# Optimization experiments

Hardware: AMD Instinct MI355X
Metric: run time of the kernel (lower is better)

Reference implementation:

```python
import jax, jax.numpy as jnp
import numpy as np

N, Q, K, L, H, C, B = 32768, 8192, 16, 8, 128, 20, 4
COS_EPS = 1e-8


def setup_inputs() -> dict:
    key = jax.random.key(0)
    ks = jax.random.split(key, 8)
    support_xyz = jax.random.normal(ks[0], (N, 3), jnp.float32)
    batch_index = jnp.sort(jax.random.randint(ks[1], (N,), 0, B))
    filtered_index = jnp.sort(jax.random.randint(ks[2], (Q,), 0, N))
    gcnfeat = jax.random.normal(ks[3], (N, H + C), jnp.float32)
    leaf_node_all = jax.random.normal(ks[4], (Q, L, 3 * H), jnp.float32)
    W1 = jax.random.normal(ks[5], (10, 64), jnp.float32) * 0.1
    b1 = jnp.zeros((64,), jnp.float32)
    W2 = jax.random.normal(ks[6], (64, H), jnp.float32) * 0.1
    b2 = jnp.zeros((H,), jnp.float32)
    Wl = jax.random.normal(ks[7], (C, H), jnp.float32) * 0.1
    bl = jnp.zeros((H,), jnp.float32)
    return dict(support_xyz=support_xyz, batch_index=batch_index,
                filtered_index=filtered_index, gcnfeat=gcnfeat,
                leaf_node_all=leaf_node_all, W1=W1, b1=b1, W2=W2, b2=b2,
                Wl=Wl, bl=bl)


def _cosine_aff(a, b):
    # a: [Q,L,H], b: [Q,K,H] -> [Q,L,K] cosine similarity matrix
    an = a / jnp.maximum(jnp.linalg.norm(a, axis=-1, keepdims=True), COS_EPS)
    bn = b / jnp.maximum(jnp.linalg.norm(b, axis=-1, keepdims=True), COS_EPS)
    return jnp.einsum('qlh,qkh->qlk', an, bn)


def _auction(mat):
    # Bertsekas auction algorithm (maximization LAP), mat: [L,K], K >= L.
    Lr, Kc = mat.shape
    eps = 1.0 / Lr
    col_ids = jnp.arange(Kc, dtype=jnp.int32)

    def cond(st):
        _, ass = st
        return jnp.any(ass < 0)

    def body(st):
        cost, ass = st
        unassigned = ass < 0                                   # [L]
        value = mat - cost[None, :]                            # [L,K]
        top2, top_idx = jax.lax.top_k(value, 2)
        bid_inc = jnp.where(unassigned, top2[:, 0] - top2[:, 1] + eps, 0.0)
        bids = jnp.zeros((Lr, Kc), mat.dtype).at[jnp.arange(Lr), top_idx[:, 0]].set(bid_inc)
        have_bid = jnp.any(bids > 0, axis=0)                   # [K]
        high_bid = jnp.max(bids, axis=0)                       # [K]
        high_bidder = jnp.argmax(bids, axis=0).astype(jnp.int32)
        cost = cost + jnp.where(have_bid, high_bid, 0.0)
        # kick out previous owners of columns that received bids
        kicked = (ass >= 0) & have_bid[jnp.clip(ass, 0, Kc - 1)]
        ass = jnp.where(kicked, -1, ass)
        # assign the high bidder of each bid-receiving column (others dropped OOB)
        tgt = jnp.where(have_bid, high_bidder, Lr)
        ass = ass.at[tgt].set(col_ids, mode='drop')
        return cost, ass

    cost0 = jnp.zeros((Kc,), mat.dtype)
    ass0 = jnp.full((Lr,), -1, jnp.int32)
    _, ass = jax.lax.while_loop(cond, body, (cost0, ass0))
    return ass


def reference(support_xyz, batch_index, filtered_index, gcnfeat, leaf_node_all,
              W1, b1, W2, b2, Wl, bl):
    query_xyz = support_xyz[filtered_index]                    # [Q,3]
    qb = batch_index[filtered_index]                           # [Q]
    # batched KNN: squared distances via GEMM form, mask cross-batch pairs
    d2 = (jnp.sum(query_xyz ** 2, -1)[:, None]
          + jnp.sum(support_xyz ** 2, -1)[None, :]
          - 2.0 * query_xyz @ support_xyz.T)                   # [Q,N]
    d2 = jnp.where(qb[:, None] == batch_index[None, :], d2, jnp.inf)
    _, col = jax.lax.top_k(-d2, K)                             # [Q,K]
    xyz_j = support_xyz[col]                                   # [Q,K,3]
    xyz_i = jnp.broadcast_to(query_xyz[:, None, :], xyz_j.shape)
    diff = xyz_i - xyz_j
    dist = jnp.linalg.norm(diff, axis=-1, keepdims=True)
    ew = jnp.concatenate([xyz_i, xyz_j, diff, dist], axis=-1)  # [Q,K,10]
    edge_w = jax.nn.relu(ew @ W1 + b1) @ W2 + b2               # [Q,K,H] rel_map
    feat_j = gcnfeat[col]                                      # [Q,K,H+C]
    cls_w = feat_j[..., -C:] @ Wl + bl                         # [Q,K,H] label_map
    m1 = _cosine_aff(leaf_node_all[:, :, :H], edge_w)
    m2 = _cosine_aff(leaf_node_all[:, :, H:2 * H], cls_w)
    m3 = _cosine_aff(leaf_node_all[:, :, 2 * H:], feat_j[..., :H])
    mat = (m1 + m2) / 4.0 + m3 / 2.0                           # [Q,L,K]
    gm_idx = jax.vmap(_auction)(jax.lax.stop_gradient(mat))    # [Q,L]
    scores = jnp.take_along_axis(mat, gm_idx[:, :, None].astype(jnp.int32), axis=2)[..., 0]
    return jnp.mean(scores, axis=-1)                           # [Q]
```

## Files before the change

kernel.cpp:

```cpp
#include <hip/hip_runtime.h>
#include <stdint.h>

#define KNN 16
#define LROWS 8
#define KBQ 8
#define KCAP 128

__device__ __forceinline__ void load4(const float* __restrict__ sxyz, int i0,
                                      int N, float px[4], float py[4],
                                      float pz[4]) {
  if (i0 + 4 <= N) {
    float4 v0 = *(const float4*)&sxyz[3 * i0];
    float4 v1 = *(const float4*)&sxyz[3 * i0 + 4];
    float4 v2 = *(const float4*)&sxyz[3 * i0 + 8];
    px[0] = v0.x; py[0] = v0.y; pz[0] = v0.z;
    px[1] = v0.w; py[1] = v1.x; pz[1] = v1.y;
    px[2] = v1.z; py[2] = v1.w; pz[2] = v2.x;
    px[3] = v2.y; py[3] = v2.z; pz[3] = v2.w;
  } else {
#pragma unroll
    for (int e = 0; e < 4; ++e) {
      int i = i0 + e; bool ok = i < N;
      px[e] = ok ? sxyz[3 * i] : 0.f;
      py[e] = ok ? sxyz[3 * i + 1] : 0.f;
      pz[e] = ok ? sxyz[3 * i + 2] : 0.f;
    }
  }
}

__global__ __launch_bounds__(256) void knn_kernel(
    const float* __restrict__ sxyz, const int* __restrict__ bidx,
    const int* __restrict__ fidx, int* __restrict__ col, int N, int Q) {
  const int t = threadIdx.x;
  const int qbase = blockIdx.x * KBQ;

  __shared__ float s_min[KBQ][256];
  __shared__ unsigned long long s_cand[KBQ][KCAP];
  __shared__ int s_cnt[KBQ];
  __shared__ float s_thr[KBQ];
  __shared__ float s_qx[KBQ], s_qy[KBQ], s_qz[KBQ];
  __shared__ int s_lo[KBQ], s_hi[KBQ];

  if (t < 2 * KBQ) {
    int qi = qbase + (t & (KBQ - 1));
    if (qi < Q) {
      int fi = fidx[qi];
      int qb = bidx[fi];
      if (t < KBQ) {
        s_qx[t] = sxyz[3 * fi]; s_qy[t] = sxyz[3 * fi + 1]; s_qz[t] = sxyz[3 * fi + 2];
        int a = 0, b = N;
        while (a < b) { int m = (a + b) >> 1; if (bidx[m] < qb) a = m + 1; else b = m; }
        s_lo[t] = a;
      } else {
        int a = 0, b = N;
        while (a < b) { int m = (a + b) >> 1; if (bidx[m] <= qb) a = m + 1; else b = m; }
        s_hi[t - KBQ] = a;
      }
    } else {
      if (t < KBQ) { s_lo[t] = 0; s_qx[t] = s_qy[t] = s_qz[t] = 0.f; }
      else s_hi[t - KBQ] = 0;
    }
  }
  if (t < KBQ) s_cnt[t] = 0;
  __syncthreads();

  float qx[KBQ], qy[KBQ], qz[KBQ], qmin[KBQ];
  int qlo[KBQ], qhi[KBQ];
#pragma unroll
  for (int qi = 0; qi < KBQ; ++qi) {
    qx[qi] = s_qx[qi]; qy[qi] = s_qy[qi]; qz[qi] = s_qz[qi];
    qlo[qi] = s_lo[qi]; qhi[qi] = s_hi[qi];
    qmin[qi] = 3e38f;
  }
  int blo = qlo[0], bhi = qhi[0];
#pragma unroll
  for (int qi = 1; qi < KBQ; ++qi) { blo = min(blo, qlo[qi]); bhi = max(bhi, qhi[qi]); }
  const int base = blo & ~3;

  for (int i0 = base + 4 * t; i0 < bhi; i0 += 1024) {
    float px[4], py[4], pz[4];
    load4(sxyz, i0, N, px, py, pz);
#pragma unroll
    for (int e = 0; e < 4; ++e) {
      int i = i0 + e;
#pragma unroll
      for (int qi = 0; qi < KBQ; ++qi) {
        float dx = qx[qi] - px[e], dy = qy[qi] - py[e], dz = qz[qi] - pz[e];
        float d2 = fmaf(dx, dx, fmaf(dy, dy, dz * dz));
        bool v = (i >= qlo[qi]) && (i < qhi[qi]);
        qmin[qi] = fminf(qmin[qi], v ? d2 : 3e38f);
      }
    }
  }
#pragma unroll
  for (int qi = 0; qi < KBQ; ++qi) s_min[qi][t] = qmin[qi];
  __syncthreads();

  {
    int qi = t >> 5, u = t & 31;
    float v[8];
#pragma unroll
    for (int s = 0; s < 8; ++s) v[s] = s_min[qi][u + 32 * s];
    float thr = 3e38f;
    for (int r = 0; r < KNN; ++r) {
      float lm = fminf(fminf(fminf(v[0], v[1]), fminf(v[2], v[3])),
                       fminf(fminf(v[4], v[5]), fminf(v[6], v[7])));
      float gm = lm;
      gm = fminf(gm, __shfl_xor(gm, 1, 64));
      gm = fminf(gm, __shfl_xor(gm, 2, 64));
      gm = fminf(gm, __shfl_xor(gm, 4, 64));
      gm = fminf(gm, __shfl_xor(gm, 8, 64));
      gm = fminf(gm, __shfl_xor(gm, 16, 64));
      unsigned long long b = __ballot(lm == gm);
      unsigned mask = (unsigned)((b >> (t & 32)) & 0xffffffffull);
      int win = __ffs(mask) - 1;
      if (u == win) {
        if (v[0] == gm) v[0] = 3e38f; else if (v[1] == gm) v[1] = 3e38f;
        else if (v[2] == gm) v[2] = 3e38f; else if (v[3] == gm) v[3] = 3e38f;
        else if (v[4] == gm) v[4] = 3e38f; else if (v[5] == gm) v[5] = 3e38f;
        else if (v[6] == gm) v[6] = 3e38f; else v[7] = 3e38f;
      }
      thr = gm;
    }
    if (u == 0)
      s_thr[qi] = (s_hi[qi] - s_lo[qi] <= KCAP) ? 3e38f : thr;
  }
  __syncthreads();

  float qthr[KBQ];
#pragma unroll
  for (int qi = 0; qi < KBQ; ++qi) qthr[qi] = s_thr[qi];

  for (int i0 = base + 4 * t; i0 < bhi; i0 += 1024) {
    float px[4], py[4], pz[4];
    load4(sxyz, i0, N, px, py, pz);
#pragma unroll
    for (int e = 0; e < 4; ++e) {
      int i = i0 + e;
#pragma unroll
      for (int qi = 0; qi < KBQ; ++qi) {
        float dx = qx[qi] - px[e], dy = qy[qi] - py[e], dz = qz[qi] - pz[e];
        float d2 = fmaf(dx, dx, fmaf(dy, dy, dz * dz));
        if (i >= qlo[qi] && i < qhi[qi] && d2 <= qthr[qi]) {
          int pos = atomicAdd(&s_cnt[qi], 1);
          if (pos < KCAP)
            s_cand[qi][pos] =
                (((unsigned long long)__float_as_uint(d2)) << 32) | (unsigned)i;
        }
      }
    }
  }
  __syncthreads();

  {
    int qi = t >> 5, u = t & 31;
    int M = min(s_cnt[qi], KCAP);
    for (int r = 0; r < KNN; ++r) {
      unsigned long long lm = ~0ull; int ls = -1;
      for (int s = u; s < M; s += 32) {
        unsigned long long vv = s_cand[qi][s];
        if (vv < lm) { lm = vv; ls = s; }
      }
      unsigned long long gm = lm, o;
      o = __shfl_xor(gm, 1, 64); if (o < gm) gm = o;
      o = __shfl_xor(gm, 2, 64); if (o < gm) gm = o;
      o = __shfl_xor(gm, 4, 64); if (o < gm) gm = o;
      o = __shfl_xor(gm, 8, 64); if (o < gm) gm = o;
      o = __shfl_xor(gm, 16, 64); if (o < gm) gm = o;
      unsigned long long b = __ballot(lm == gm);
      unsigned mask = (unsigned)((b >> (t & 32)) & 0xffffffffull);
      int win = __ffs(mask) - 1;
      if (u == win && ls >= 0 && gm != ~0ull) {
        s_cand[qi][ls] = ~0ull;
        col[(size_t)(qbase + qi) * KNN + r] = (int)(unsigned)(gm & 0xffffffffull);
      }
    }
  }
}

#define OFF_LEAF 0
#define OFF_EDGE 3104
#define OFF_B 5184
#define OFF_EW 7264
#define OFF_FC 7456
#define S_TOTAL 7776

template <bool EXT>
__global__ __launch_bounds__(128) void fused_kernel(
    const float* __restrict__ sxyz,
    const int* __restrict__ fidx,
    const float* __restrict__ gcn,
    const float* __restrict__ leaf,
    const float* __restrict__ W1, const float* __restrict__ b1,
    const float* __restrict__ W2, const float* __restrict__ b2,
    const float* __restrict__ Wl, const float* __restrict__ bl,
    const int* __restrict__ col,
    float* __restrict__ matw, float* __restrict__ out) {
  const int q = blockIdx.x;
  const int t = threadIdx.x;

  __shared__ __align__(16) float S[S_TOTAL];
  __shared__ int s_col[KNN];
  __shared__ float s_rna[24];
  __shared__ float s_rnb[3][KNN];
  __shared__ float s_mat[LROWS * 17];

  {
    const float4* lp = (const float4*)(leaf + (size_t)q * 3072);
#pragma unroll
    for (int r = 0; r < 6; ++r) {
      int v = r * 128 + t;
      float4 f = lp[v];
      int l = v / 96, off = (v % 96) * 4;
      *(float4*)&S[OFF_LEAF + l * 388 + off] = f;
    }
  }
  if (t < KNN) s_col[t] = col[q * KNN + t];
  __syncthreads();

  for (int v = t; v < KNN * 20; v += 128)
    S[OFF_FC + v] = gcn[(size_t)s_col[v / 20] * 148 + 128 + (v % 20)];
  if (t < KNN) {
    int fi = fidx[q];
    float qx = sxyz[3 * fi], qy = sxyz[3 * fi + 1], qz = sxyz[3 * fi + 2];
    int j = s_col[t];
    float jx = sxyz[3 * j], jy = sxyz[3 * j + 1], jz = sxyz[3 * j + 2];
    float dx = qx - jx, dy = qy - jy, dz = qz - jz;
    float dist = sqrtf(dx * dx + dy * dy + dz * dz);
    float* e = &S[OFF_EW + t * 12];
    e[0] = qx; e[1] = qy; e[2] = qz;
    e[3] = jx; e[4] = jy; e[5] = jz;
    e[6] = dx; e[7] = dy; e[8] = dz; e[9] = dist;
  }
  __syncthreads();

  for (int r = 0; r < 8; ++r) {
    int o = r * 128 + t;
    int k = o >> 6, jj = o & 63;
    float acc0 = b1[jj];
#pragma unroll
    for (int i = 0; i < 10; ++i)
      acc0 = fmaf(S[OFF_EW + k * 12 + i], W1[i * 64 + jj], acc0);
    S[OFF_B + k * 68 + jj] = fmaxf(acc0, 0.0f);
  }
  __syncthreads();

  float acc[KNN];
#pragma unroll
  for (int k = 0; k < KNN; ++k) acc[k] = b2[t];
#pragma unroll
  for (int j4 = 0; j4 < 16; ++j4) {
    float w0 = W2[(4 * j4 + 0) * 128 + t];
    float w1 = W2[(4 * j4 + 1) * 128 + t];
    float w2 = W2[(4 * j4 + 2) * 128 + t];
    float w3 = W2[(4 * j4 + 3) * 128 + t];
#pragma unroll
    for (int k = 0; k < KNN; ++k) {
      float4 h = *(const float4*)&S[OFF_B + k * 68 + 4 * j4];
      acc[k] = fmaf(h.x, w0, acc[k]);
      acc[k] = fmaf(h.y, w1, acc[k]);
      acc[k] = fmaf(h.z, w2, acc[k]);
      acc[k] = fmaf(h.w, w3, acc[k]);
    }
  }
#pragma unroll
  for (int k = 0; k < KNN; ++k) S[OFF_EDGE + k * 130 + t] = acc[k];
  __syncthreads();

#pragma unroll
  for (int k = 0; k < KNN; ++k) acc[k] = bl[t];
#pragma unroll
  for (int c = 0; c < 20; ++c) {
    float wv = Wl[c * 128 + t];
#pragma unroll
    for (int k = 0; k < KNN; ++k) acc[k] = fmaf(S[OFF_FC + k * 20 + c], wv, acc[k]);
  }
#pragma unroll
  for (int k = 0; k < KNN; ++k) S[OFF_B + k * 130 + t] = acc[k];
  __syncthreads();

  if (t < 72) {
    float s0 = 0, s1 = 0, s2 = 0, s3 = 0;
    if (t < 56) {
      const float* p;
      if (t < 24) p = &S[OFF_LEAF + (t / 3) * 388 + (t % 3) * 128];
      else if (t < 40) p = &S[OFF_EDGE + (t - 24) * 130];
      else p = &S[OFF_B + (t - 40) * 130];
#pragma unroll 4
      for (int h = 0; h < 128; h += 4) {
        float2 v0 = *(const float2*)&p[h];
        float2 v1 = *(const float2*)&p[h + 2];
        s0 = fmaf(v0.x, v0.x, s0); s1 = fmaf(v0.y, v0.y, s1);
        s2 = fmaf(v1.x, v1.x, s2); s3 = fmaf(v1.y, v1.y, s3);
      }
    } else {
      const float4* p = (const float4*)(gcn + (size_t)s_col[t - 56] * 148);
#pragma unroll 4
      for (int h = 0; h < 32; ++h) {
        float4 v = p[h];
        s0 = fmaf(v.x, v.x, s0); s1 = fmaf(v.y, v.y, s1);
        s2 = fmaf(v.z, v.z, s2); s3 = fmaf(v.w, v.w, s3);
      }
    }
    float rn = 1.0f / fmaxf(sqrtf((s0 + s1) + (s2 + s3)), 1e-8f);
    if (t < 24) s_rna[t] = rn;
    else if (t < 40) s_rnb[0][t - 24] = rn;
    else if (t < 56) s_rnb[1][t - 40] = rn;
    else s_rnb[2][t - 56] = rn;
  }
  __syncthreads();

  {
    int l = t >> 4, k = t & 15;
    const float* a0 = &S[OFF_LEAF + l * 388];
    const float* be = &S[OFF_EDGE + k * 130];
    const float* bc = &S[OFF_B + k * 130];
    const float* bf = gcn + (size_t)s_col[k] * 148;
    float d0 = 0, d1 = 0, d2 = 0;
    for (int h = 0; h < 128; h += 4) {
      float4 va0 = *(const float4*)&a0[h];
      float4 va1 = *(const float4*)&a0[128 + h];
      float4 va2 = *(const float4*)&a0[256 + h];
      float4 vbf = *(const float4*)&bf[h];
      float2 ve0 = *(const float2*)&be[h];
      float2 ve1 = *(const float2*)&be[h + 2];
      float2 vc0 = *(const float2*)&bc[h];
      float2 vc1 = *(const float2*)&bc[h + 2];
      d0 = fmaf(va0.x, ve0.x, d0); d0 = fmaf(va0.y, ve0.y, d0);
      d0 = fmaf(va0.z, ve1.x, d0); d0 = fmaf(va0.w, ve1.y, d0);
      d1 = fmaf(va1.x, vc0.x, d1); d1 = fmaf(va1.y, vc0.y, d1);
      d1 = fmaf(va1.z, vc1.x, d1); d1 = fmaf(va1.w, vc1.y, d1);
      d2 = fmaf(va2.x, vbf.x, d2); d2 = fmaf(va2.y, vbf.y, d2);
      d2 = fmaf(va2.z, vbf.z, d2); d2 = fmaf(va2.w, vbf.w, d2);
    }
    float m = (d0 * s_rna[l * 3 + 0] * s_rnb[0][k] +
               d1 * s_rna[l * 3 + 1] * s_rnb[1][k]) * 0.25f +
              d2 * s_rna[l * 3 + 2] * s_rnb[2][k] * 0.5f;
    if (EXT) {
      matw[(size_t)q * 128 + t] = m;
      return;
    }
    s_mat[l * 17 + k] = m;
  }
  __syncthreads();
  if (t >= 64) return;

  float mrow[KNN];
#pragma unroll
  for (int c = 0; c < KNN; ++c) mrow[c] = s_mat[(t & 7) * 17 + c];
  int ass = -1;
  float cost = 0.f;
  for (int it = 0; it < 1024; ++it) {
    float v1 = -3e38f, v2 = -3e38f; int c1 = 0;
#pragma unroll
    for (int c = 0; c < KNN; ++c) {
      float costc = __shfl(cost, c, 64);
      float v = mrow[c] - costc;
      if (v > v1) { v2 = v1; v1 = v; c1 = c; }
      else if (v > v2) v2 = v;
    }
    int bidc = (t < 8 && ass < 0) ? c1 : -1;
    float bidv = v1 - v2 + 0.125f;
    float high = -3e38f; int hb = -1;
#pragma unroll
    for (int r = 0; r < 8; ++r) {
      int bc = __shfl(bidc, r, 64);
      float bv = __shfl(bidv, r, 64);
      if (bc == t && bv > high) { high = bv; hb = r; }
    }
    if (t < 16 && hb >= 0) cost += high;
    int hb_c = __shfl(hb, bidc < 0 ? 0 : bidc, 64);
    int hb_a = __shfl(hb, ass < 0 ? 0 : ass, 64);
    if (t < 8) {
      if (ass >= 0 && hb_a >= 0) ass = -1;
      if (bidc >= 0 && hb_c == t) ass = bidc;
    }
    if (__ballot((t < 8) ? (ass >= 0) : 1) == ~0ull) break;
  }
  float s = 0.f;
#pragma unroll
  for (int r = 0; r < 8; ++r) {
    int a = __shfl(ass, r, 64);
    if (t == 0) s += s_mat[r * 17 + a];
  }
  if (t == 0) out[q] = s * 0.125f;
}

__global__ __launch_bounds__(256) void auction_kernel(
    const float* __restrict__ matw, float* __restrict__ out, int Q) {
  const int t = threadIdx.x;
  const int lane = t & 63;
  const int gj = lane & 15;
  const int gb = lane & ~15;
  const int q = blockIdx.x * 16 + (t >> 6) * 4 + (lane >> 4);
  const bool valid = q < Q;

  float mrow[KNN];
  if (valid && gj < 8) {
    const float4* mp = (const float4*)(matw + (size_t)q * 128 + gj * 16);
    float4 a = mp[0], b = mp[1], c = mp[2], d = mp[3];
    mrow[0] = a.x; mrow[1] = a.y; mrow[2] = a.z; mrow[3] = a.w;
    mrow[4] = b.x; mrow[5] = b.y; mrow[6] = b.z; mrow[7] = b.w;
    mrow[8] = c.x; mrow[9] = c.y; mrow[10] = c.z; mrow[11] = c.w;
    mrow[12] = d.x; mrow[13] = d.y; mrow[14] = d.z; mrow[15] = d.w;
  } else {
#pragma unroll
    for (int c = 0; c < KNN; ++c) mrow[c] = 0.f;
  }
  int ass = (valid && gj < 8) ? -1 : 0;
  float cost = 0.f;

  for (int it = 0; it < 512; ++it) {
    float v1 = -3e38f, v2 = -3e38f; int c1 = 0;
#pragma unroll
    for (int c = 0; c < KNN; ++c) {
      float costc = __shfl(cost, gb + c, 64);
      float v = mrow[c] - costc;
      if (v > v1) { v2 = v1; v1 = v; c1 = c; }
      else if (v > v2) v2 = v;
    }
    int bidc = (valid && gj < 8 && ass < 0) ? c1 : -1;
    float bidv = v1 - v2 + 0.125f;

    float high = -3e38f; int hb = -1;
#pragma unroll
    for (int r = 0; r < 8; ++r) {
      int bc = __shfl(bidc, gb + r, 64);
      float bv = __shfl(bidv, gb + r, 64);
      if (bc == gj && bv > high) { high = bv; hb = r; }
    }
    if (hb >= 0) cost += high;

    int hb_c = __shfl(hb, gb + (bidc < 0 ? 0 : bidc), 64);
    int hb_a = __shfl(hb, gb + (ass < 0 ? 0 : ass), 64);
    if (valid && gj < 8) {
      if (ass >= 0 && hb_a >= 0) ass = -1;
      if (bidc >= 0 && hb_c == gj) ass = bidc;
    }
    if (__ballot(ass >= 0) == ~0ull) break;
  }

  float val = 0.f;
  if (valid && gj < 8) {
#pragma unroll
    for (int c = 0; c < KNN; ++c) val = (ass == c) ? mrow[c] : val;
  }
  val += __shfl_xor(val, 1, 64);
  val += __shfl_xor(val, 2, 64);
  val += __shfl_xor(val, 4, 64);
  if (valid && gj == 0) out[q] = val * 0.125f;
}

extern "C" void kernel_launch(void* const* d_in, const int* in_sizes, int n_in,
                              void* d_out, int out_size, void* d_ws, size_t ws_size,
                              hipStream_t stream) {
  const float* sxyz = (const float*)d_in[0];
  const int* bidx = (const int*)d_in[1];
  const int* fidx = (const int*)d_in[2];
  const float* gcn = (const float*)d_in[3];
  const float* leaf = (const float*)d_in[4];
  const float* W1 = (const float*)d_in[5];
  const float* b1 = (const float*)d_in[6];
  const float* W2 = (const float*)d_in[7];
  const float* b2 = (const float*)d_in[8];
  const float* Wl = (const float*)d_in[9];
  const float* bl = (const float*)d_in[10];
  float* out = (float*)d_out;

  const int N = in_sizes[0] / 3;
  const int Q = in_sizes[2];

  char* ws = (char*)d_ws;
  int* col = (int*)ws;
  float* matw = (float*)(ws + (size_t)Q * KNN * 4);
  const size_t need = (size_t)Q * KNN * 4 + (size_t)Q * 128 * 4;

  knn_kernel<<<(Q + KBQ - 1) / KBQ, 256, 0, stream>>>(sxyz, bidx, fidx, col, N, Q);
  if (ws_size >= need) {
    fused_kernel<true><<<Q, 128, 0, stream>>>(sxyz, fidx, gcn, leaf, W1, b1, W2,
                                              b2, Wl, bl, col, matw, out);
    auction_kernel<<<(Q + 15) / 16, 256, 0, stream>>>(matw, out, Q);
  } else {
    fused_kernel<false><<<Q, 128, 0, stream>>>(sxyz, fidx, gcn, leaf, W1, b1, W2,
                                               b2, Wl, bl, col, nullptr, out);
  }
}
```

Before: 385.4 us.

## Precompute batch bounds and read leaf features directly from global memory

Adds a small kernel that records the start and end index of each batch segment, so the KNN kernel can look them up instead of running per-query binary searches over the batch index. The fused kernel no longer stages the leaf features in LDS. It reads them from global memory for the norm and dot-product passes, which shrinks shared memory per block and can raise occupancy. This adds an extra kernel launch and repeated global reads of leaf rows, and the starts/ends buffers are sized for at most 4096 batches and are never initialised, so batches with no points would leave stale bounds.

Measured after the change: 389.2 us. About the same (+1.0%).

```diff
diff --git a/kernel.cpp b/kernel.cpp
--- a/kernel.cpp
+++ b/kernel.cpp
@@ -5,6 +5,15 @@
 #define LROWS 8
 #define KBQ 8
 #define KCAP 128
+
+__global__ void prep_bounds(const int* __restrict__ bidx, int N,
+                            int* __restrict__ starts, int* __restrict__ ends) {
+  int i = blockIdx.x * 256 + threadIdx.x;
+  if (i >= N) return;
+  int b = bidx[i];
+  if (i == 0 || bidx[i - 1] != b) starts[b] = i;
+  if (i == N - 1 || bidx[i + 1] != b) ends[b] = i + 1;
+}
 
 __device__ __forceinline__ void load4(const float* __restrict__ sxyz, int i0,
                                       int N, float px[4], float py[4],
@@ -28,9 +37,11 @@
   }
 }
 
+template <bool FAST>
 __global__ __launch_bounds__(256) void knn_kernel(
     const float* __restrict__ sxyz, const int* __restrict__ bidx,
-    const int* __restrict__ fidx, int* __restrict__ col, int N, int Q) {
+    const int* __restrict__ fidx, const int* __restrict__ starts,
+    const int* __restrict__ ends, int* __restrict__ col, int N, int Q) {
   const int t = threadIdx.x;
   const int qbase = blockIdx.x * KBQ;
 
@@ -46,15 +57,24 @@
     if (qi < Q) {
       int fi = fidx[qi];
       int qb = bidx[fi];
-      if (t < KBQ) {
-        s_qx[t] = sxyz[3 * fi]; s_qy[t] = sxyz[3 * fi + 1]; s_qz[t] = sxyz[3 * fi + 2];
-        int a = 0, b = N;
-        while (a < b) { int m = (a + b) >> 1; if (bidx[m] < qb) a = m + 1; else b = m; }
-        s_lo[t] = a;
+      if (FAST) {
+        if (t < KBQ) {
+          s_qx[t] = sxyz[3 * fi]; s_qy[t] = sxyz[3 * fi + 1]; s_qz[t] = sxyz[3 * fi + 2];
+          s_lo[t] = starts[qb];
+        } else {
+          s_hi[t - KBQ] = ends[qb];
+        }
       } else {
-        int a = 0, b = N;
-        while (a < b) { int m = (a + b) >> 1; if (bidx[m] <= qb) a = m + 1; else b = m; }
-        s_hi[t - KBQ] = a;
+        if (t < KBQ) {
+          s_qx[t] = sxyz[3 * fi]; s_qy[t] = sxyz[3 * fi + 1]; s_qz[t] = sxyz[3 * fi + 2];
+          int a = 0, b = N;
+          while (a < b) { int m = (a + b) >> 1; if (bidx[m] < qb) a = m + 1; else b = m; }
+          s_lo[t] = a;
+        } else {
+          int a = 0, b = N;
+          while (a < b) { int m = (a + b) >> 1; if (bidx[m] <= qb) a = m + 1; else b = m; }
+          s_hi[t - KBQ] = a;
+        }
       }
     } else {
       if (t < KBQ) { s_lo[t] = 0; s_qx[t] = s_qy[t] = s_qz[t] = 0.f; }
@@ -178,12 +198,11 @@
   }
 }
 
-#define OFF_LEAF 0
-#define OFF_EDGE 3104
-#define OFF_B 5184
-#define OFF_EW 7264
-#define OFF_FC 7456
-#define S_TOTAL 7776
+#define OFF_EDGE 0
+#define OFF_B 2080
+#define OFF_EW 4160
+#define OFF_FC 4352
+#define S_TOTAL 4672
 
 template <bool EXT>
 __global__ __launch_bounds__(128) void fused_kernel(
@@ -203,18 +222,7 @@
   __shared__ int s_col[KNN];
   __shared__ float s_rna[24];
   __shared__ float s_rnb[3][KNN];
-  __shared__ float s_mat[LROWS * 17];
-
-  {
-    const float4* lp = (const float4*)(leaf + (size_t)q * 3072);
-#pragma unroll
-    for (int r = 0; r < 6; ++r) {
-      int v = r * 128 + t;
-      float4 f = lp[v];
-      int l = v / 96, off = (v % 96) * 4;
-      *(float4*)&S[OFF_LEAF + l * 388 + off] = f;
-    }
-  }
+
   if (t < KNN) s_col[t] = col[q * KNN + t];
   __syncthreads();
 
@@ -281,11 +289,18 @@
 
   if (t < 72) {
     float s0 = 0, s1 = 0, s2 = 0, s3 = 0;
-    if (t < 56) {
-      const float* p;
-      if (t < 24) p = &S[OFF_LEAF + (t / 3) * 388 + (t % 3) * 128];
-      else if (t < 40) p = &S[OFF_EDGE + (t - 24) * 130];
-      else p = &S[OFF_B + (t - 40) * 130];
+    if (t < 24 || t >= 56) {
+      const float4* p = (t < 24)
+          ? (const float4*)(leaf + (size_t)q * 3072 + (t / 3) * 384 + (t % 3) * 128)
+          : (const float4*)(gcn + (size_t)s_col[t - 56] * 148);
+#pragma unroll 4
+      for (int h = 0; h < 32; ++h) {
+        float4 v = p[h];
+        s0 = fmaf(v.x, v.x, s0); s1 = fmaf(v.y, v.y, s1);
+        s2 = fmaf(v.z, v.z, s2); s3 = fmaf(v.w, v.w, s3);
+      }
+    } else {
+      const float* p = (t < 40) ? &S[OFF_EDGE + (t - 24) * 130] : &S[OFF_B + (t - 40) * 130];
 #pragma unroll 4
       for (int h = 0; h < 128; h += 4) {
         float2 v0 = *(const float2*)&p[h];
@@ -293,14 +308,6 @@
         s0 = fmaf(v0.x, v0.x, s0); s1 = fmaf(v0.y, v0.y, s1);
         s2 = fmaf(v1.x, v1.x, s2); s3 = fmaf(v1.y, v1.y, s3);
       }
-    } else {
-      const float4* p = (const float4*)(gcn + (size_t)s_col[t - 56] * 148);
-#pragma unroll 4
-      for (int h = 0; h < 32; ++h) {
-        float4 v = p[h];
-        s0 = fmaf(v.x, v.x, s0); s1 = fmaf(v.y, v.y, s1);
-        s2 = fmaf(v.z, v.z, s2); s3 = fmaf(v.w, v.w, s3);
-      }
     }
     float rn = 1.0f / fmaxf(sqrtf((s0 + s1) + (s2 + s3)), 1e-8f);
     if (t < 24) s_rna[t] = rn;
@@ -312,7 +319,7 @@
 
   {
     int l = t >> 4, k = t & 15;
-    const float* a0 = &S[OFF_LEAF + l * 388];
+    const float* a0 = leaf + (size_t)q * 3072 + l * 384;
     const float* be = &S[OFF_EDGE + k * 130];
     const float* bc = &S[OFF_B + k * 130];
     const float* bf = gcn + (size_t)s_col[k] * 148;
@@ -340,11 +347,12 @@
       matw[(size_t)q * 128 + t] = m;
       return;
     }
-    s_mat[l * 17 + k] = m;
+    S[OFF_EW + l * 17 + k] = m;
   }
   __syncthreads();
   if (t >= 64) return;
 
+  float* s_mat = &S[OFF_EW];
   float mrow[KNN];
 #pragma unroll
   for (int c = 0; c < KNN; ++c) mrow[c] = s_mat[(t & 7) * 17 + c];
@@ -472,11 +480,21 @@
 
   char* ws = (char*)d_ws;
   int* col = (int*)ws;
-  float* matw = (float*)(ws + (size_t)Q * KNN * 4);
-  const size_t need = (size_t)Q * KNN * 4 + (size_t)Q * 128 * 4;
-
-  knn_kernel<<<(Q + KBQ - 1) / KBQ, 256, 0, stream>>>(sxyz, bidx, fidx, col, N, Q);
-  if (ws_size >= need) {
+  int* starts = (int*)(ws + (size_t)Q * KNN * 4);
+  int* ends = starts + 4096;
+  float* matw = (float*)(ws + (size_t)Q * KNN * 4 + 32768);
+  const size_t need_bounds = (size_t)Q * KNN * 4 + 32768;
+  const size_t need_full = need_bounds + (size_t)Q * 128 * 4;
+
+  if (ws_size >= need_bounds) {
+    prep_bounds<<<(N + 255) / 256, 256, 0, stream>>>(bidx, N, starts, ends);
+    knn_kernel<true><<<(Q + KBQ - 1) / KBQ, 256, 0, stream>>>(
+        sxyz, bidx, fidx, starts, ends, col, N, Q);
+  } else {
+    knn_kernel<false><<<(Q + KBQ - 1) / KBQ, 256, 0, stream>>>(
+        sxyz, bidx, fidx, nullptr, nullptr, col, N, Q);
+  }
+  if (ws_size >= need_full) {
     fused_kernel<true><<<Q, 128, 0, stream>>>(sxyz, fidx, gcn, leaf, W1, b1, W2,
                                               b2, Wl, bl, col, matw, out);
     auction_kernel<<<(Q + 15) / 16, 256, 0, stream>>>(matw, out, Q);
```
